# Optimization experiments

Hardware: AMD Instinct MI355X
Metric: run time of the kernel (lower is better)

Reference implementation:

```python
import jax, jax.numpy as jnp
import numpy as np

DIM = 1024
NUM_HEADS = 16
HEAD_DIM = DIM // NUM_HEADS

def setup_inputs() -> dict:
    key = jax.random.key(0)
    ks = jax.random.split(key, 5)
    s = 1.0 / np.sqrt(DIM)
    x = jax.random.normal(ks[0], (2, 2048, DIM), dtype=jnp.float32)
    W_qkv = jax.random.uniform(ks[1], (DIM, 3 * DIM), dtype=jnp.float32, minval=-s, maxval=s)
    b_qkv = jax.random.uniform(ks[2], (3 * DIM,), dtype=jnp.float32, minval=-s, maxval=s)
    W_out = jax.random.uniform(ks[3], (DIM, DIM), dtype=jnp.float32, minval=-s, maxval=s)
    b_out = jax.random.uniform(ks[4], (DIM,), dtype=jnp.float32, minval=-s, maxval=s)
    return {"x": x, "W_qkv": W_qkv, "b_qkv": b_qkv, "W_out": W_out, "b_out": b_out}

def reference(x, W_qkv, b_qkv, W_out, b_out):
    B, S, _ = x.shape
    qkv = x @ W_qkv + b_qkv                       # [B,S,3*dim]
    q, k, v = jnp.split(qkv, 3, axis=-1)
    # [B,S,dim] -> [B,H,S,hd]
    def to_heads(t):
        return t.reshape(B, S, NUM_HEADS, HEAD_DIM).transpose(0, 2, 1, 3)
    q, k, v = to_heads(q), to_heads(k), to_heads(v)
    scale = HEAD_DIM ** -0.5
    scores = jnp.einsum('bhqd,bhkd->bhqk', q, k) * scale
    attn = jax.nn.softmax(scores, axis=-1)
    out = jnp.einsum('bhqk,bhkd->bhqd', attn, v)  # [B,H,S,hd]
    out = out.transpose(0, 2, 1, 3).reshape(B, S, DIM)
    return out @ W_out + b_out
```

## Files before the change

### kernel.cpp

```cpp
#include <hip/hip_runtime.h>
#include <math.h>

#define DIMM    1024
#define NHEADS  16
#define HDIM    64
#define BATCH   2
#define SEQ     2048
#define ROWS    (BATCH*SEQ)

typedef _Float16 f16x8 __attribute__((ext_vector_type(8)));
typedef _Float16 f16x4 __attribute__((ext_vector_type(4)));
typedef float    f32x4 __attribute__((ext_vector_type(4)));

__device__ inline void gl_lds16(const void* g, void* l) {
    __builtin_amdgcn_global_load_lds(
        (const __attribute__((address_space(1))) void*)g,
        (__attribute__((address_space(3))) void*)l, 16, 0, 0);
}

__device__ void tcvt64(const float* __restrict__ in, _Float16* __restrict__ out,
                       int K, int N, int k0, int n0, float (*tile)[65], int t)
{
    {
        const int c4 = (t & 15) * 4;
        const int r  = t >> 4;
        #pragma unroll
        for (int i = 0; i < 4; i++) {
            const int rr = r + 16 * i;
            float4 v = *(const float4*)(in + (size_t)(k0 + rr) * N + n0 + c4);
            tile[rr][c4] = v.x; tile[rr][c4 + 1] = v.y;
            tile[rr][c4 + 2] = v.z; tile[rr][c4 + 3] = v.w;
        }
    }
    __syncthreads();
    #pragma unroll
    for (int i = 0; i < 2; i++) {
        const int seg = t + 256 * i;
        const int n   = seg >> 3;
        const int kc  = (seg & 7) * 8;
        f16x8 o;
        #pragma unroll
        for (int j = 0; j < 8; j++) o[j] = (_Float16)tile[kc + j][n];
        *(f16x8*)(out + (size_t)(n0 + n) * K + k0 + kc) = o;
    }
}

__global__ __launch_bounds__(256)
void prep_kernel(const float* __restrict__ x, const float* __restrict__ Wqkv,
                 const float* __restrict__ Wout, _Float16* __restrict__ xh,
                 _Float16* __restrict__ wqkvt, _Float16* __restrict__ woutt)
{
    __shared__ float tile[64][65];
    const int bx = blockIdx.x;
    const int t  = threadIdx.x;
    if (bx < 2048) {
        const int i = bx * 256 + t;
        const float4 a = *(const float4*)(x + (size_t)i * 8);
        const float4 b = *(const float4*)(x + (size_t)i * 8 + 4);
        f16x8 o;
        o[0] = (_Float16)a.x; o[1] = (_Float16)a.y; o[2] = (_Float16)a.z; o[3] = (_Float16)a.w;
        o[4] = (_Float16)b.x; o[5] = (_Float16)b.y; o[6] = (_Float16)b.z; o[7] = (_Float16)b.w;
        *(f16x8*)(xh + (size_t)i * 8) = o;
    } else if (bx < 2816) {
        const int id = bx - 2048;
        const int gx = id % 48, gy = id / 48;
        tcvt64(Wqkv, wqkvt, DIMM, 3 * DIMM, gy * 64, gx * 64, tile, t);
    } else {
        const int id = bx - 2816;
        const int gx = id & 15, gy = id >> 4;
        tcvt64(Wout, woutt, DIMM, DIMM, gy * 64, gx * 64, tile, t);
    }
}

__global__ __launch_bounds__(256)
void vtranspose_kernel(const _Float16* __restrict__ qkvh, _Float16* __restrict__ vt)
{
    __shared__ _Float16 tile[64][72];
    const int kt = blockIdx.x;
    const int bh = blockIdx.y;
    const int b  = bh >> 4, h = bh & 15;
    const int t  = threadIdx.x;
    {
        const int key = t >> 2, c4 = (t & 3) * 16;
        const _Float16* src = qkvh + ((size_t)(b * SEQ + kt * 64 + key)) * (3 * DIMM)
                              + 2 * DIMM + h * HDIM + c4;
        f16x8 v0 = *(const f16x8*)src;
        f16x8 v1 = *(const f16x8*)(src + 8);
        #pragma unroll
        for (int j = 0; j < 8; j++) {
            tile[c4 + j][key]     = v0[j];
            tile[c4 + 8 + j][key] = v1[j];
        }
    }
    __syncthreads();
    {
        const int d = t >> 2, k4 = (t & 3) * 16;
        f16x8 o0, o1;
        #pragma unroll
        for (int j = 0; j < 8; j++) { o0[j] = tile[d][k4 + j]; o1[j] = tile[d][k4 + 8 + j]; }
        _Float16* dst = vt + ((size_t)bh * 64 + d) * SEQ + kt * 64 + k4;
        *(f16x8*)dst       = o0;
        *(f16x8*)(dst + 8) = o1;
    }
}

template<int OUT_F16>
__global__ __launch_bounds__(256)
void hgemm_bias_kernel(const _Float16* __restrict__ A, const _Float16* __restrict__ Bt,
                       const float* __restrict__ bias, void* __restrict__ Cout,
                       int N, int K)
{
    __shared__ _Float16 As[128 * 64];
    __shared__ _Float16 Bs[128 * 64];

    const int t    = threadIdx.x;
    const int w    = t >> 6, lane = t & 63;
    const int quad = lane >> 4, l16 = lane & 15;
    const int wr   = w >> 1, wc = w & 1;
    const int row0 = blockIdx.y * 128, col0 = blockIdx.x * 128;
    const int sw   = l16 & 7;

    f32x4 acc[4][4];
    #pragma unroll
    for (int i = 0; i < 4; i++)
        #pragma unroll
        for (int j = 0; j < 4; j++)
            #pragma unroll
            for (int r = 0; r < 4; r++) acc[i][j][r] = 0.f;

    const _Float16* gA[4];
    const _Float16* gB[4];
    int lofs[4];
    #pragma unroll
    for (int j = 0; j < 4; j++) {
        const int s   = t + 256 * j;
        const int row = s >> 3;
        const int kb  = (s & 7) ^ (row & 7);
        gA[j] = A  + (size_t)(row0 + row) * K + kb * 8;
        gB[j] = Bt + (size_t)(col0 + row) * K + kb * 8;
        lofs[j] = s * 8;
    }

    const int niter = K >> 6;
    #pragma unroll 1
    for (int it = 0; it < niter; it++) {
        __syncthreads();
        #pragma unroll
        for (int j = 0; j < 4; j++) gl_lds16(gA[j], As + lofs[j]);
        #pragma unroll
        for (int j = 0; j < 4; j++) gl_lds16(gB[j], Bs + lofs[j]);
        #pragma unroll
        for (int j = 0; j < 4; j++) { gA[j] += 64; gB[j] += 64; }
        __syncthreads();

        f16x8 af[4][2], bf[4][2];
        #pragma unroll
        for (int i = 0; i < 4; i++) {
            const int arow = wr * 64 + i * 16 + l16;
            const int brow = wc * 64 + i * 16 + l16;
            #pragma unroll
            for (int hh = 0; hh < 2; hh++) {
                af[i][hh] = *(const f16x8*)(As + (arow * 8 + ((hh * 4 + quad) ^ sw)) * 8);
                bf[i][hh] = *(const f16x8*)(Bs + (brow * 8 + ((hh * 4 + quad) ^ sw)) * 8);
            }
        }
        #pragma unroll
        for (int i = 0; i < 4; i++)
            #pragma unroll
            for (int j = 0; j < 4; j++) {
                acc[i][j] = __builtin_amdgcn_mfma_f32_16x16x32_f16(af[i][0], bf[j][0], acc[i][j], 0, 0, 0);
                acc[i][j] = __builtin_amdgcn_mfma_f32_16x16x32_f16(af[i][1], bf[j][1], acc[i][j], 0, 0, 0);
            }
    }

    #pragma unroll
    for (int j = 0; j < 4; j++) {
        const int col = col0 + wc * 64 + j * 16 + l16;
        const float bv = bias[col];
        #pragma unroll
        for (int i = 0; i < 4; i++) {
            const int row = row0 + wr * 64 + i * 16 + quad * 4;
            #pragma unroll
            for (int r = 0; r < 4; r++) {
                const float v = acc[i][j][r] + bv;
                if (OUT_F16)
                    ((_Float16*)Cout)[(size_t)(row + r) * N + col] = (_Float16)v;
                else
                    ((float*)Cout)[(size_t)(row + r) * N + col] = v;
            }
        }
    }
}

__global__ __launch_bounds__(256, 4)
void flash_attn_kernel(const _Float16* __restrict__ qkv,
                       const _Float16* __restrict__ vtg,
                       _Float16* __restrict__ out)
{
    const int qt = blockIdx.x;
    const int bh = blockIdx.y;
    const int b  = bh >> 4, h = bh & 15;
    const int t    = threadIdx.x;
    const int w    = t >> 6;
    const int lane = t & 63;
    const int quad = lane >> 4;
    const int l16  = lane & 15;
    const int sw   = l16 & 7;

    __shared__ __align__(16) _Float16 Ks [64 * 64];
    __shared__ __align__(16) _Float16 Vts[64 * 64];
    __shared__ __align__(16) _Float16 Ps [64 * 72];

    const int q0 = qt * 64;
    const size_t rstr = 3 * DIMM;
    const _Float16* qbase = qkv + (size_t)b * SEQ * rstr;

    f16x8 qf[4][2];
    #pragma unroll
    for (int qb = 0; qb < 4; qb++) {
        const _Float16* qrow = qbase + (size_t)(q0 + qb * 16 + l16) * rstr + h * HDIM;
        qf[qb][0] = *(const f16x8*)(qrow + quad * 8);
        qf[qb][1] = *(const f16x8*)(qrow + 32 + quad * 8);
    }

    f32x4 Oacc[4];
    #pragma unroll
    for (int i = 0; i < 4; i++) Oacc[i] = (f32x4){0.f, 0.f, 0.f, 0.f};
    float lrow[4] = {0.f, 0.f, 0.f, 0.f};

    const int seg0 = t, seg1 = t + 256;
    const int r0 = seg0 >> 3, lb0 = (seg0 & 7) ^ (r0 & 7);
    const int r1 = seg1 >> 3, lb1 = (seg1 & 7) ^ (r1 & 7);
    const _Float16* gK0 = qbase + (size_t)r0 * rstr + DIMM + h * HDIM + lb0 * 8;
    const _Float16* gK1 = qbase + (size_t)r1 * rstr + DIMM + h * HDIM + lb1 * 8;
    const _Float16* gV0 = vtg + ((size_t)bh * 64 + r0) * SEQ + lb0 * 8;
    const _Float16* gV1 = vtg + ((size_t)bh * 64 + r1) * SEQ + lb1 * 8;

    const int kAbase = (16 * w + l16) * 64;
    const int pAbase = (16 * w + l16) * 72;

    #pragma unroll 1
    for (int k0 = 0; k0 < SEQ; k0 += 64) {
        __syncthreads();
        gl_lds16(gK0 + (size_t)k0 * rstr, Ks  + seg0 * 8);
        gl_lds16(gK1 + (size_t)k0 * rstr, Ks  + seg1 * 8);
        gl_lds16(gV0 + k0,                Vts + seg0 * 8);
        gl_lds16(gV1 + k0,                Vts + seg1 * 8);
        __syncthreads();

        f16x8 kf0 = *(const f16x8*)(Ks + kAbase + ((0 + quad) ^ sw) * 8);
        f16x8 kf1 = *(const f16x8*)(Ks + kAbase + ((4 + quad) ^ sw) * 8);
        #pragma unroll
        for (int qb = 0; qb < 4; qb++) {
            f32x4 s = (f32x4){0.f, 0.f, 0.f, 0.f};
            s = __builtin_amdgcn_mfma_f32_16x16x32_f16(kf0, qf[qb][0], s, 0, 0, 0);
            s = __builtin_amdgcn_mfma_f32_16x16x32_f16(kf1, qf[qb][1], s, 0, 0, 0);
            float p0 = __expf(s[0] * 0.125f);
            float p1 = __expf(s[1] * 0.125f);
            float p2 = __expf(s[2] * 0.125f);
            float p3 = __expf(s[3] * 0.125f);
            lrow[qb] += (p0 + p1) + (p2 + p3);
            f16x4 pk;
            pk[0] = (_Float16)p0; pk[1] = (_Float16)p1;
            pk[2] = (_Float16)p2; pk[3] = (_Float16)p3;
            *(f16x4*)(Ps + (qb * 16 + l16) * 72 + 16 * w + 4 * quad) = pk;
        }
        __syncthreads();

        f16x8 pf0 = *(const f16x8*)(Ps + pAbase + quad * 8);
        f16x8 pf1 = *(const f16x8*)(Ps + pAbase + 32 + quad * 8);
        #pragma unroll
        for (int db = 0; db < 4; db++) {
            const int vrow = db * 16 + l16;
            f16x8 vf0 = *(const f16x8*)(Vts + vrow * 64 + ((0 + quad) ^ sw) * 8);
            f16x8 vf1 = *(const f16x8*)(Vts + vrow * 64 + ((4 + quad) ^ sw) * 8);
            Oacc[db] = __builtin_amdgcn_mfma_f32_16x16x32_f16(pf0, vf0, Oacc[db], 0, 0, 0);
            Oacc[db] = __builtin_amdgcn_mfma_f32_16x16x32_f16(pf1, vf1, Oacc[db], 0, 0, 0);
        }
    }

    #pragma unroll
    for (int qb = 0; qb < 4; qb++) {
        lrow[qb] += __shfl_xor(lrow[qb], 16);
        lrow[qb] += __shfl_xor(lrow[qb], 32);
    }
    __syncthreads();
    float* lbuf = (float*)Ks;
    if (lane < 16) {
        #pragma unroll
        for (int qb = 0; qb < 4; qb++) lbuf[w * 64 + qb * 16 + lane] = lrow[qb];
    }
    __syncthreads();
    const int qloc = 16 * w + quad * 4;
    float lrec[4];
    #pragma unroll
    for (int r = 0; r < 4; r++) {
        const int q = qloc + r;
        lrec[r] = 1.f / (lbuf[q] + lbuf[64 + q] + lbuf[128 + q] + lbuf[192 + q]);
    }
    #pragma unroll
    for (int db = 0; db < 4; db++) {
        #pragma unroll
        for (int r = 0; r < 4; r++) {
            out[(size_t)(b * SEQ + q0 + qloc + r) * DIMM + h * HDIM + db * 16 + l16] =
                (_Float16)(Oacc[db][r] * lrec[r]);
        }
    }
}

extern "C" void kernel_launch(void* const* d_in, const int* in_sizes, int n_in,
                              void* d_out, int out_size, void* d_ws, size_t ws_size,
                              hipStream_t stream)
{
    const float* x    = (const float*)d_in[0];
    const float* Wqkv = (const float*)d_in[1];
    const float* bqkv = (const float*)d_in[2];
    const float* Wout = (const float*)d_in[3];
    const float* bout = (const float*)d_in[4];
    float* out = (float*)d_out;

    _Float16* qkvh  = (_Float16*)d_ws;
    _Float16* attnh = qkvh  + (size_t)ROWS * 3 * DIMM;
    _Float16* xh    = attnh + (size_t)ROWS * DIMM;
    _Float16* wqkvt = xh    + (size_t)ROWS * DIMM;
    _Float16* woutt = wqkvt + (size_t)3 * DIMM * DIMM;
    _Float16* vtg   = woutt + (size_t)DIMM * DIMM;

    prep_kernel<<<3072, 256, 0, stream>>>(x, Wqkv, Wout, xh, wqkvt, woutt);
    {
        dim3 grid(3 * DIMM / 128, ROWS / 128);
        hgemm_bias_kernel<1><<<grid, 256, 0, stream>>>(xh, wqkvt, bqkv, qkvh, 3 * DIMM, DIMM);
    }
    {
        dim3 grid(SEQ / 64, BATCH * NHEADS);
        vtranspose_kernel<<<grid, 256, 0, stream>>>(qkvh, vtg);
    }
    {
        dim3 grid(SEQ / 64, BATCH * NHEADS);
        flash_attn_kernel<<<grid, 256, 0, stream>>>(qkvh, vtg, attnh);
    }
    {
        dim3 grid(DIMM / 128, ROWS / 128);
        hgemm_bias_kernel<0><<<grid, 256, 0, stream>>>(attnh, woutt, bout, out, DIMM, DIMM);
    }
}
```

Baseline: 206.3 us.

## Fuse V transpose into QKV GEMM epilogue and double query tile in flash attention

```diff
diff --git a/kernel.cpp b/kernel.cpp
--- a/kernel.cpp
+++ b/kernel.cpp
@@ -72,43 +72,11 @@
     }
 }
 
-__global__ __launch_bounds__(256)
-void vtranspose_kernel(const _Float16* __restrict__ qkvh, _Float16* __restrict__ vt)
-{
-    __shared__ _Float16 tile[64][72];
-    const int kt = blockIdx.x;
-    const int bh = blockIdx.y;
-    const int b  = bh >> 4, h = bh & 15;
-    const int t  = threadIdx.x;
-    {
-        const int key = t >> 2, c4 = (t & 3) * 16;
-        const _Float16* src = qkvh + ((size_t)(b * SEQ + kt * 64 + key)) * (3 * DIMM)
-                              + 2 * DIMM + h * HDIM + c4;
-        f16x8 v0 = *(const f16x8*)src;
-        f16x8 v1 = *(const f16x8*)(src + 8);
-        #pragma unroll
-        for (int j = 0; j < 8; j++) {
-            tile[c4 + j][key]     = v0[j];
-            tile[c4 + 8 + j][key] = v1[j];
-        }
-    }
-    __syncthreads();
-    {
-        const int d = t >> 2, k4 = (t & 3) * 16;
-        f16x8 o0, o1;
-        #pragma unroll
-        for (int j = 0; j < 8; j++) { o0[j] = tile[d][k4 + j]; o1[j] = tile[d][k4 + 8 + j]; }
-        _Float16* dst = vt + ((size_t)bh * 64 + d) * SEQ + kt * 64 + k4;
-        *(f16x8*)dst       = o0;
-        *(f16x8*)(dst + 8) = o1;
-    }
-}
-
-template<int OUT_F16>
+template<int MODE>
 __global__ __launch_bounds__(256)
 void hgemm_bias_kernel(const _Float16* __restrict__ A, const _Float16* __restrict__ Bt,
                        const float* __restrict__ bias, void* __restrict__ Cout,
-                       int N, int K)
+                       _Float16* __restrict__ vtg, int N, int K)
 {
     __shared__ _Float16 As[128 * 64];
     __shared__ _Float16 Bs[128 * 64];
@@ -173,6 +141,7 @@
             }
     }
 
+    const bool vblock = (MODE == 1) && (col0 >= 2 * DIMM);
     #pragma unroll
     for (int j = 0; j < 4; j++) {
         const int col = col0 + wc * 64 + j * 16 + l16;
@@ -180,19 +149,29 @@
         #pragma unroll
         for (int i = 0; i < 4; i++) {
             const int row = row0 + wr * 64 + i * 16 + quad * 4;
-            #pragma unroll
-            for (int r = 0; r < 4; r++) {
-                const float v = acc[i][j][r] + bv;
-                if (OUT_F16)
-                    ((_Float16*)Cout)[(size_t)(row + r) * N + col] = (_Float16)v;
-                else
-                    ((float*)Cout)[(size_t)(row + r) * N + col] = v;
-            }
-        }
-    }
-}
-
-__global__ __launch_bounds__(256, 4)
+            if (vblock) {
+                const int dg  = col - 2 * DIMM;
+                const int h   = dg >> 6, dl = dg & 63;
+                const int b   = row >> 11, key = row & (SEQ - 1);
+                f16x4 o;
+                #pragma unroll
+                for (int r = 0; r < 4; r++) o[r] = (_Float16)(acc[i][j][r] + bv);
+                *(f16x4*)(vtg + ((size_t)((b * NHEADS + h) * 64 + dl)) * SEQ + key) = o;
+            } else {
+                #pragma unroll
+                for (int r = 0; r < 4; r++) {
+                    const float v = acc[i][j][r] + bv;
+                    if (MODE == 1)
+                        ((_Float16*)Cout)[(size_t)(row + r) * N + col] = (_Float16)v;
+                    else
+                        ((float*)Cout)[(size_t)(row + r) * N + col] = v;
+                }
+            }
+        }
+    }
+}
+
+__global__ __launch_bounds__(256, 2)
 void flash_attn_kernel(const _Float16* __restrict__ qkv,
                        const _Float16* __restrict__ vtg,
                        _Float16* __restrict__ out)
@@ -209,24 +188,28 @@
 
     __shared__ __align__(16) _Float16 Ks [64 * 64];
     __shared__ __align__(16) _Float16 Vts[64 * 64];
-    __shared__ __align__(16) _Float16 Ps [64 * 72];
-
-    const int q0 = qt * 64;
+    __shared__ __align__(16) _Float16 Ps [128 * 72];
+
+    const int q0 = qt * 128;
     const size_t rstr = 3 * DIMM;
     const _Float16* qbase = qkv + (size_t)b * SEQ * rstr;
 
-    f16x8 qf[4][2];
-    #pragma unroll
-    for (int qb = 0; qb < 4; qb++) {
+    f16x8 qf[8][2];
+    #pragma unroll
+    for (int qb = 0; qb < 8; qb++) {
         const _Float16* qrow = qbase + (size_t)(q0 + qb * 16 + l16) * rstr + h * HDIM;
         qf[qb][0] = *(const f16x8*)(qrow + quad * 8);
         qf[qb][1] = *(const f16x8*)(qrow + 32 + quad * 8);
     }
 
-    f32x4 Oacc[4];
-    #pragma unroll
-    for (int i = 0; i < 4; i++) Oacc[i] = (f32x4){0.f, 0.f, 0.f, 0.f};
-    float lrow[4] = {0.f, 0.f, 0.f, 0.f};
+    f32x4 Oacc[2][4];
+    #pragma unroll
+    for (int ss = 0; ss < 2; ss++)
+        #pragma unroll
+        for (int i = 0; i < 4; i++) Oacc[ss][i] = (f32x4){0.f, 0.f, 0.f, 0.f};
+    float lrow[8];
+    #pragma unroll
+    for (int qb = 0; qb < 8; qb++) lrow[qb] = 0.f;
 
     const int seg0 = t, seg1 = t + 256;
     const int r0 = seg0 >> 3, lb0 = (seg0 & 7) ^ (r0 & 7);
@@ -237,7 +220,6 @@
     const _Float16* gV1 = vtg + ((size_t)bh * 64 + r1) * SEQ + lb1 * 8;
 
     const int kAbase = (16 * w + l16) * 64;
-    const int pAbase = (16 * w + l16) * 72;
 
     #pragma unroll 1
     for (int k0 = 0; k0 < SEQ; k0 += 64) {
@@ -251,7 +233,7 @@
         f16x8 kf0 = *(const f16x8*)(Ks + kAbase + ((0 + quad) ^ sw) * 8);
         f16x8 kf1 = *(const f16x8*)(Ks + kAbase + ((4 + quad) ^ sw) * 8);
         #pragma unroll
-        for (int qb = 0; qb < 4; qb++) {
+        for (int qb = 0; qb < 8; qb++) {
             f32x4 s = (f32x4){0.f, 0.f, 0.f, 0.f};
             s = __builtin_amdgcn_mfma_f32_16x16x32_f16(kf0, qf[qb][0], s, 0, 0, 0);
             s = __builtin_amdgcn_mfma_f32_16x16x32_f16(kf1, qf[qb][1], s, 0, 0, 0);
@@ -267,20 +249,28 @@
         }
         __syncthreads();
 
-        f16x8 pf0 = *(const f16x8*)(Ps + pAbase + quad * 8);
-        f16x8 pf1 = *(const f16x8*)(Ps + pAbase + 32 + quad * 8);
+        f16x8 vf[4][2];
         #pragma unroll
         for (int db = 0; db < 4; db++) {
             const int vrow = db * 16 + l16;
-            f16x8 vf0 = *(const f16x8*)(Vts + vrow * 64 + ((0 + quad) ^ sw) * 8);
-            f16x8 vf1 = *(const f16x8*)(Vts + vrow * 64 + ((4 + quad) ^ sw) * 8);
-            Oacc[db] = __builtin_amdgcn_mfma_f32_16x16x32_f16(pf0, vf0, Oacc[db], 0, 0, 0);
-            Oacc[db] = __builtin_amdgcn_mfma_f32_16x16x32_f16(pf1, vf1, Oacc[db], 0, 0, 0);
-        }
-    }
-
-    #pragma unroll
-    for (int qb = 0; qb < 4; qb++) {
+            vf[db][0] = *(const f16x8*)(Vts + vrow * 64 + ((0 + quad) ^ sw) * 8);
+            vf[db][1] = *(const f16x8*)(Vts + vrow * 64 + ((4 + quad) ^ sw) * 8);
+        }
+        #pragma unroll
+        for (int ss = 0; ss < 2; ss++) {
+            const int prow = ((2 * w + ss) * 16 + l16) * 72;
+            f16x8 pf0 = *(const f16x8*)(Ps + prow + quad * 8);
+            f16x8 pf1 = *(const f16x8*)(Ps + prow + 32 + quad * 8);
+            #pragma unroll
+            for (int db = 0; db < 4; db++) {
+                Oacc[ss][db] = __builtin_amdgcn_mfma_f32_16x16x32_f16(pf0, vf[db][0], Oacc[ss][db], 0, 0, 0);
+                Oacc[ss][db] = __builtin_amdgcn_mfma_f32_16x16x32_f16(pf1, vf[db][1], Oacc[ss][db], 0, 0, 0);
+            }
+        }
+    }
+
+    #pragma unroll
+    for (int qb = 0; qb < 8; qb++) {
         lrow[qb] += __shfl_xor(lrow[qb], 16);
         lrow[qb] += __shfl_xor(lrow[qb], 32);
     }
@@ -288,22 +278,25 @@
     float* lbuf = (float*)Ks;
     if (lane < 16) {
         #pragma unroll
-        for (int qb = 0; qb < 4; qb++) lbuf[w * 64 + qb * 16 + lane] = lrow[qb];
+        for (int qb = 0; qb < 8; qb++) lbuf[w * 128 + qb * 16 + lane] = lrow[qb];
     }
     __syncthreads();
-    const int qloc = 16 * w + quad * 4;
-    float lrec[4];
-    #pragma unroll
-    for (int r = 0; r < 4; r++) {
-        const int q = qloc + r;
-        lrec[r] = 1.f / (lbuf[q] + lbuf[64 + q] + lbuf[128 + q] + lbuf[192 + q]);
-    }
-    #pragma unroll
-    for (int db = 0; db < 4; db++) {
+    #pragma unroll
+    for (int ss = 0; ss < 2; ss++) {
+        const int qloc = 32 * w + ss * 16 + quad * 4;
+        float lrec[4];
         #pragma unroll
         for (int r = 0; r < 4; r++) {
-            out[(size_t)(b * SEQ + q0 + qloc + r) * DIMM + h * HDIM + db * 16 + l16] =
-                (_Float16)(Oacc[db][r] * lrec[r]);
+            const int q = qloc + r;
+            lrec[r] = 1.f / (lbuf[q] + lbuf[128 + q] + lbuf[256 + q] + lbuf[384 + q]);
+        }
+        #pragma unroll
+        for (int db = 0; db < 4; db++) {
+            #pragma unroll
+            for (int r = 0; r < 4; r++) {
+                out[(size_t)(b * SEQ + q0 + qloc + r) * DIMM + h * HDIM + db * 16 + l16] =
+                    (_Float16)(Oacc[ss][db][r] * lrec[r]);
+            }
         }
     }
 }
@@ -329,18 +322,14 @@
     prep_kernel<<<3072, 256, 0, stream>>>(x, Wqkv, Wout, xh, wqkvt, woutt);
     {
         dim3 grid(3 * DIMM / 128, ROWS / 128);
-        hgemm_bias_kernel<1><<<grid, 256, 0, stream>>>(xh, wqkvt, bqkv, qkvh, 3 * DIMM, DIMM);
+        hgemm_bias_kernel<1><<<grid, 256, 0, stream>>>(xh, wqkvt, bqkv, qkvh, vtg, 3 * DIMM, DIMM);
     }
     {
-        dim3 grid(SEQ / 64, BATCH * NHEADS);
-        vtranspose_kernel<<<grid, 256, 0, stream>>>(qkvh, vtg);
-    }
-    {
-        dim3 grid(SEQ / 64, BATCH * NHEADS);
+        dim3 grid(SEQ / 128, BATCH * NHEADS);
         flash_attn_kernel<<<grid, 256, 0, stream>>>(qkvh, vtg, attnh);
     }
     {
         dim3 grid(DIMM / 128, ROWS / 128);
-        hgemm_bias_kernel<0><<<grid, 256, 0, stream>>>(attnh, woutt, bout, out, DIMM, DIMM);
-    }
-}
+        hgemm_bias_kernel<0><<<grid, 256, 0, stream>>>(attnh, woutt, bout, out, nullptr, DIMM, DIMM);
+    }
+}
```

Result: slower. 213.1 us (+3.3%).
